# Optimization experiments

Measured on AMD Instinct MI355X. Metric: run time of the kernel, lower is better.

The kernel has to match this reference:

```python
import jax, jax.numpy as jnp
import numpy as np

EMBED_DIM = 1024
NUM_HEADS = 16
HEAD_DIM = EMBED_DIM // NUM_HEADS
B, T = 4, 2048


def setup_inputs() -> dict:
    key = jax.random.key(0)
    ks = jax.random.split(key, 11)
    s = 1.0 / np.sqrt(EMBED_DIM)
    return {
        "query": jax.random.normal(ks[0], (B, T, EMBED_DIM), jnp.float32),
        "key_in": jax.random.normal(ks[1], (B, T, EMBED_DIM), jnp.float32),
        "value": jax.random.normal(ks[2], (B, T, EMBED_DIM), jnp.float32),
        "Wq": jax.random.normal(ks[3], (EMBED_DIM, EMBED_DIM), jnp.float32) * s,
        "bq": jnp.zeros((EMBED_DIM,), jnp.float32),
        "Wk": jax.random.normal(ks[4], (EMBED_DIM, EMBED_DIM), jnp.float32) * s,
        "bk": jnp.zeros((EMBED_DIM,), jnp.float32),
        "Wv": jax.random.normal(ks[5], (EMBED_DIM, EMBED_DIM), jnp.float32) * s,
        "bv": jnp.zeros((EMBED_DIM,), jnp.float32),
        "Wo": jax.random.normal(ks[6], (EMBED_DIM, EMBED_DIM), jnp.float32) * s,
        "bo": jnp.zeros((EMBED_DIM,), jnp.float32),
    }


def reference(query, key_in, value, Wq, bq, Wk, bk, Wv, bv, Wo, bo):
    # nn.Linear: x @ W.T + b
    def split_heads(x):  # [B,T,D] -> [B,H,T,hd]
        return x.reshape(B, T, NUM_HEADS, HEAD_DIM).transpose(0, 2, 1, 3)

    q = split_heads(query @ Wq.T + bq)
    k = split_heads(key_in @ Wk.T + bk)
    v = split_heads(value @ Wv.T + bv)
    scores = jnp.einsum("bhqd,bhkd->bhqk", q, k) / jnp.sqrt(jnp.float32(HEAD_DIM))
    attn = jax.nn.softmax(scores, axis=-1)
    out = jnp.einsum("bhqk,bhkd->bhqd", attn, v)
    out = out.transpose(0, 2, 1, 3).reshape(B, T, EMBED_DIM)
    return out @ Wo.T + bo
```

## Files before the change

### kernel.cpp

```cpp
#include <hip/hip_runtime.h>
#include <hip/hip_bf16.h>
#include <stdint.h>

typedef __bf16 bf16;
typedef __bf16 bf16x8 __attribute__((ext_vector_type(8)));
typedef float f32x4 __attribute__((ext_vector_type(4)));

#define BATCH 4
#define SEQ   2048
#define DIM   1024
#define NH    16
#define HD    64

#define QSCALE 0.18033688011112042f

#define MFMA(a, b, c) __builtin_amdgcn_mfma_f32_16x16x32_bf16((a), (b), (c), 0, 0, 0)

#define GLOAD16(gsrc, ldst)                                                        \
  __builtin_amdgcn_global_load_lds(                                                \
      (__attribute__((address_space(1))) unsigned int*)(void*)(gsrc),              \
      (__attribute__((address_space(3))) unsigned int*)(ldst), 16, 0, 0)

static __device__ __forceinline__ float fast_exp2(float x) {
#if __has_builtin(__builtin_amdgcn_exp2f)
  return __builtin_amdgcn_exp2f(x);
#else
  return exp2f(x);
#endif
}

__global__ __launch_bounds__(256) void cvt_w_kernel(
    const float* __restrict__ w0, const float* __restrict__ w1,
    const float* __restrict__ w2, const float* __restrict__ w3,
    bf16* __restrict__ o0, bf16* __restrict__ o1,
    bf16* __restrict__ o2, bf16* __restrict__ o3) {
  const float* s;
  bf16* d;
  switch (blockIdx.y) {
    case 0: s = w0; d = o0; break;
    case 1: s = w1; d = o1; break;
    case 2: s = w2; d = o2; break;
    default: s = w3; d = o3; break;
  }
  const int i = (blockIdx.x * 256 + threadIdx.x) * 4;
  const float4 v = *(const float4*)(s + i);
  ushort4 o;
  o.x = __builtin_bit_cast(unsigned short, (bf16)v.x);
  o.y = __builtin_bit_cast(unsigned short, (bf16)v.y);
  o.z = __builtin_bit_cast(unsigned short, (bf16)v.z);
  o.w = __builtin_bit_cast(unsigned short, (bf16)v.w);
  *(ushort4*)((unsigned short*)d + i) = o;
}

struct ProjArgs {
  const float* A[3];
  const bf16*  W[3];
  const float* bias[3];
  bf16*        out[3];
};

__global__ __launch_bounds__(256, 3) void proj_gemm(ProjArgs p) {
  const int z = blockIdx.z;
  const float* __restrict__ A    = p.A[z];
  const bf16*  __restrict__ W    = p.W[z];
  const float* __restrict__ bias = p.bias[z];
  bf16*        __restrict__ out  = p.out[z];

  __shared__ float Af[128 * 64];
  __shared__ bf16  Bb[128 * 64];

  const int tid  = threadIdx.x;
  const int wave = tid >> 6, lane = tid & 63;
  const int r = lane & 15, g = lane >> 4;

  const int wg = blockIdx.x;
  const int sw = ((wg & 7) << 6) | (wg >> 3);
  const int m0 = (sw >> 3) * 128, n0 = (sw & 7) * 128;
  const int wm = (wave >> 1) * 64, wn = (wave & 1) * 64;

  f32x4 acc[4][4] = {};

  const int a_sr = lane >> 4;
  const int a_cb = (lane & 15) * 16;
  const int b_sr = lane >> 3;
  const int b_cb = (lane & 7) * 16;

  const int NK = DIM / 64;
  for (int it = 0; it < NK; ++it) {
    const int k0 = it * 64;

#pragma unroll
    for (int i = 0; i < 8; ++i) {
      const int row = wave * 32 + i * 4 + a_sr;
      const char* src = (const char*)(A + (size_t)(m0 + row) * DIM + k0) +
                        (a_cb ^ ((row & 15) << 4));
      GLOAD16(src, (char*)Af + (wave * 32 + i * 4) * 256);
    }
#pragma unroll
    for (int i = 0; i < 4; ++i) {
      const int row = wave * 32 + i * 8 + b_sr;
      const char* src = (const char*)(W + (size_t)(n0 + row) * DIM + k0) +
                        (b_cb ^ ((row & 7) << 4));
      GLOAD16(src, (char*)Bb + (wave * 32 + i * 8) * 128);
    }
    __syncthreads();

#pragma unroll
    for (int ks = 0; ks < 2; ++ks) {
      bf16x8 af[4], bfr[4];
#pragma unroll
      for (int mt = 0; mt < 4; ++mt) {
        const int mr = wm + mt * 16 + r;
        const char* base = (const char*)Af + mr * 256;
        const int asw = (mr & 15) << 4;
        const f32x4 lo = *(const f32x4*)(base + ((ks * 128 + g * 32) ^ asw));
        const f32x4 hi = *(const f32x4*)(base + ((ks * 128 + g * 32 + 16) ^ asw));
        bf16x8 a;
        a[0] = (bf16)lo[0]; a[1] = (bf16)lo[1]; a[2] = (bf16)lo[2]; a[3] = (bf16)lo[3];
        a[4] = (bf16)hi[0]; a[5] = (bf16)hi[1]; a[6] = (bf16)hi[2]; a[7] = (bf16)hi[3];
        af[mt] = a;
      }
#pragma unroll
      for (int nt = 0; nt < 4; ++nt) {
        const int nr = wn + nt * 16 + r;
        bfr[nt] = *(bf16x8*)((char*)Bb + nr * 128 +
                             ((ks * 64 + g * 16) ^ ((nr & 7) << 4)));
      }
#pragma unroll
      for (int mt = 0; mt < 4; ++mt)
#pragma unroll
        for (int nt = 0; nt < 4; ++nt)
          acc[mt][nt] = MFMA(af[mt], bfr[nt], acc[mt][nt]);
    }

    __syncthreads();
  }

  if (z == 2) {
#pragma unroll
    for (int nt = 0; nt < 4; ++nt) {
      const int n = n0 + wn + nt * 16 + r;
      const float bn = bias[n];
#pragma unroll
      for (int mt = 0; mt < 4; ++mt) {
        const int m = m0 + wm + mt * 16 + g * 4;
        const int b = m >> 11, t = m & 2047;
        ushort4 pk;
        pk.x = __builtin_bit_cast(unsigned short, (bf16)(acc[mt][nt][0] + bn));
        pk.y = __builtin_bit_cast(unsigned short, (bf16)(acc[mt][nt][1] + bn));
        pk.z = __builtin_bit_cast(unsigned short, (bf16)(acc[mt][nt][2] + bn));
        pk.w = __builtin_bit_cast(unsigned short, (bf16)(acc[mt][nt][3] + bn));
        *(ushort4*)((unsigned short*)out + (((size_t)(b * DIM + n)) << 11) + t) = pk;
      }
    }
  } else {
    const float scale = (z == 0) ? QSCALE : 1.0f;
#pragma unroll
    for (int mt = 0; mt < 4; ++mt)
#pragma unroll
      for (int nt = 0; nt < 4; ++nt) {
        const int n = n0 + wn + nt * 16 + r;
        const float bn = bias[n];
#pragma unroll
        for (int i = 0; i < 4; ++i) {
          const int m = m0 + wm + mt * 16 + g * 4 + i;
          out[(size_t)m * DIM + n] = (bf16)((acc[mt][nt][i] + bn) * scale);
        }
      }
  }
}

__global__ __launch_bounds__(256, 3) void attn_kernel(
    const bf16* __restrict__ Q, const bf16* __restrict__ K,
    const bf16* __restrict__ Vt, bf16* __restrict__ ctx) {
  __shared__ bf16 Kb[2][64 * 64];
  __shared__ bf16 Vb[2][64 * 64];
  __shared__ bf16 Pb[4][32 * 64];

  const int tid  = threadIdx.x;
  const int wave = tid >> 6, lane = tid & 63;
  const int r = lane & 15, g = lane >> 4;
  const int bh = blockIdx.y;
  const int b = bh >> 4, h = bh & 15;
  const int q0 = blockIdx.x * 128 + wave * 32;

  bf16x8 qf[2][2];
  {
    const bf16* qp = Q + ((size_t)(b * SEQ + q0 + r) * DIM + h * HD);
#pragma unroll
    for (int qt = 0; qt < 2; ++qt)
#pragma unroll
      for (int ks = 0; ks < 2; ++ks)
        qf[qt][ks] = *(const bf16x8*)(qp + (size_t)qt * 16 * DIM + ks * 32 + g * 8);
  }

  f32x4 accO[2][4] = {};
  float m_i[2] = {-3e38f, -3e38f};
  float l_i[2] = {0.f, 0.f};

  const bf16* Kbase = K + (size_t)(b * SEQ) * DIM + h * HD;
  const bf16* Vbase = Vt + (size_t)(b * DIM + h * HD) * SEQ;

  const int srr = lane >> 3;
  const int scb = (lane & 7) * 16;
  const int swz = srr << 4;

#define STAGE(buf, kv0)                                                             \
  do {                                                                              \
    _Pragma("unroll") for (int i_ = 0; i_ < 2; ++i_) {                              \
      const int row_ = wave * 16 + i_ * 8 + srr;                                    \
      const char* ks_ =                                                             \
          (const char*)(Kbase + (size_t)((kv0) + row_) * DIM) + (scb ^ swz);        \
      GLOAD16(ks_, (char*)&Kb[buf][0] + (wave * 16 + i_ * 8) * 128);                \
      const char* vs_ =                                                             \
          (const char*)(Vbase + (size_t)row_ * SEQ + (kv0)) + (scb ^ swz);          \
      GLOAD16(vs_, (char*)&Vb[buf][0] + (wave * 16 + i_ * 8) * 128);                \
    }                                                                               \
  } while (0)

  STAGE(0, 0);
  __syncthreads();

  const int NIT = SEQ / 64;
  for (int it = 0; it < NIT; ++it) {
    const int cur = it & 1;
    if (it + 1 < NIT) STAGE(cur ^ 1, (it + 1) * 64);

    f32x4 s[2][4];
#pragma unroll
    for (int qt = 0; qt < 2; ++qt)
#pragma unroll
      for (int nt = 0; nt < 4; ++nt) s[qt][nt] = f32x4{0.f, 0.f, 0.f, 0.f};
#pragma unroll
    for (int nt = 0; nt < 4; ++nt) {
      const int kr = nt * 16 + r;
#pragma unroll
      for (int ks = 0; ks < 2; ++ks) {
        const bf16x8 kf = *(bf16x8*)((char*)&Kb[cur][0] + kr * 128 +
                                     ((ks * 64 + g * 16) ^ ((kr & 7) << 4)));
        s[0][nt] = MFMA(kf, qf[0][ks], s[0][nt]);
        s[1][nt] = MFMA(kf, qf[1][ks], s[1][nt]);
      }
    }

    float pm[2];
#pragma unroll
    for (int qt = 0; qt < 2; ++qt) {
      f32x4 m4;
#pragma unroll
      for (int i = 0; i < 4; ++i)
        m4[i] = fmaxf(fmaxf(s[qt][0][i], s[qt][1][i]), fmaxf(s[qt][2][i], s[qt][3][i]));
      float t = fmaxf(fmaxf(m4[0], m4[1]), fmaxf(m4[2], m4[3]));
      t = fmaxf(t, __shfl_xor(t, 16));
      t = fmaxf(t, __shfl_xor(t, 32));
      pm[qt] = t;
    }

    const bool need = (pm[0] > m_i[0] + 8.0f) || (pm[1] > m_i[1] + 8.0f);
    if (__any(need)) {
      float alpha[2];
#pragma unroll
      for (int qt = 0; qt < 2; ++qt) {
        const float mn = fmaxf(m_i[qt], pm[qt]);
        alpha[qt] = fast_exp2(m_i[qt] - mn);
        m_i[qt] = mn;
        l_i[qt] *= alpha[qt];
      }
#pragma unroll
      for (int qt = 0; qt < 2; ++qt)
#pragma unroll
        for (int i = 0; i < 4; ++i) {
          const float a = __shfl(alpha[qt], g * 4 + i);
#pragma unroll
          for (int dt = 0; dt < 4; ++dt) accO[qt][dt][i] *= a;
        }
    }

    float rs[2] = {0.f, 0.f};
#pragma unroll
    for (int qt = 0; qt < 2; ++qt) {
      const int row = qt * 16 + r;
      const int rsw = (row & 7) << 4;
#pragma unroll
      for (int nt = 0; nt < 4; ++nt) {
        f32x4 pv;
#pragma unroll
        for (int i = 0; i < 4; ++i) {
          pv[i] = fast_exp2(s[qt][nt][i] - m_i[qt]);
          rs[qt] += pv[i];
        }
        ushort4 pk;
        pk.x = __builtin_bit_cast(unsigned short, (bf16)pv[0]);
        pk.y = __builtin_bit_cast(unsigned short, (bf16)pv[1]);
        pk.z = __builtin_bit_cast(unsigned short, (bf16)pv[2]);
        pk.w = __builtin_bit_cast(unsigned short, (bf16)pv[3]);
        *(ushort4*)((char*)&Pb[wave][0] + row * 128 + ((nt * 32 + g * 8) ^ rsw)) = pk;
      }
      rs[qt] += __shfl_xor(rs[qt], 16);
      rs[qt] += __shfl_xor(rs[qt], 32);
      l_i[qt] += rs[qt];
    }

#pragma unroll
    for (int ss = 0; ss < 2; ++ss) {
      bf16x8 pf[2];
#pragma unroll
      for (int qt = 0; qt < 2; ++qt) {
        const int row = qt * 16 + r;
        pf[qt] = *(bf16x8*)((char*)&Pb[wave][0] + row * 128 +
                            ((ss * 64 + g * 16) ^ ((row & 7) << 4)));
      }
#pragma unroll
      for (int dt = 0; dt < 4; ++dt) {
        const int dr = dt * 16 + r;
        const bf16x8 vf = *(bf16x8*)((char*)&Vb[cur][0] + dr * 128 +
                                     ((ss * 64 + g * 16) ^ ((dr & 7) << 4)));
        accO[0][dt] = MFMA(pf[0], vf, accO[0][dt]);
        accO[1][dt] = MFMA(pf[1], vf, accO[1][dt]);
      }
    }

    __syncthreads();
  }
#undef STAGE

#pragma unroll
  for (int qt = 0; qt < 2; ++qt)
#pragma unroll
    for (int i = 0; i < 4; ++i) {
      const float li = __shfl(l_i[qt], g * 4 + i);
      const float inv = 1.0f / li;
      const int qrow = q0 + qt * 16 + g * 4 + i;
      bf16* cp = ctx + (size_t)(b * SEQ + qrow) * DIM + h * HD;
#pragma unroll
      for (int dt = 0; dt < 4; ++dt)
        cp[dt * 16 + r] = (bf16)(accO[qt][dt][i] * inv);
    }
}

__global__ __launch_bounds__(256, 2) void out_gemm(
    const bf16* __restrict__ A, const bf16* __restrict__ W,
    const float* __restrict__ bias, float* __restrict__ out) {
  __shared__ bf16 Ab[2][128 * 64];
  __shared__ bf16 Bb[2][128 * 64];

  const int tid  = threadIdx.x;
  const int wave = tid >> 6, lane = tid & 63;
  const int r = lane & 15, g = lane >> 4;

  const int wg = blockIdx.x;
  const int sw = ((wg & 7) << 6) | (wg >> 3);
  const int m0 = (sw >> 3) * 128, n0 = (sw & 7) * 128;
  const int wm = (wave >> 1) * 64, wn = (wave & 1) * 64;

  f32x4 acc[4][4] = {};

  const int srr = lane >> 3;
  const int scb = (lane & 7) * 16;
  const int swz = srr << 4;

#define STAGE2(buf, k0)                                                             \
  do {                                                                              \
    _Pragma("unroll") for (int i_ = 0; i_ < 4; ++i_) {                              \
      const int row_ = wave * 32 + i_ * 8 + srr;                                    \
      const char* as_ =                                                             \
          (const char*)(A + (size_t)(m0 + row_) * DIM + (k0)) + (scb ^ swz);        \
      GLOAD16(as_, (char*)&Ab[buf][0] + (wave * 32 + i_ * 8) * 128);                \
      const char* bs_ =                                                             \
          (const char*)(W + (size_t)(n0 + row_) * DIM + (k0)) + (scb ^ swz);        \
      GLOAD16(bs_, (char*)&Bb[buf][0] + (wave * 32 + i_ * 8) * 128);                \
    }                                                                               \
  } while (0)

  STAGE2(0, 0);
  __syncthreads();

  const int NK = DIM / 64;
  for (int it = 0; it < NK; ++it) {
    const int cur = it & 1;
    if (it + 1 < NK) STAGE2(cur ^ 1, (it + 1) * 64);

#pragma unroll
    for (int ks = 0; ks < 2; ++ks) {
      bf16x8 af[4], bfr[4];
#pragma unroll
      for (int mt = 0; mt < 4; ++mt) {
        const int mr = wm + mt * 16 + r;
        af[mt] = *(bf16x8*)((char*)&Ab[cur][0] + mr * 128 +
                            ((ks * 64 + g * 16) ^ ((mr & 7) << 4)));
      }
#pragma unroll
      for (int nt = 0; nt < 4; ++nt) {
        const int nr = wn + nt * 16 + r;
        bfr[nt] = *(bf16x8*)((char*)&Bb[cur][0] + nr * 128 +
                             ((ks * 64 + g * 16) ^ ((nr & 7) << 4)));
      }
#pragma unroll
      for (int mt = 0; mt < 4; ++mt)
#pragma unroll
        for (int nt = 0; nt < 4; ++nt)
          acc[mt][nt] = MFMA(af[mt], bfr[nt], acc[mt][nt]);
    }

    __syncthreads();
  }
#undef STAGE2

#pragma unroll
  for (int mt = 0; mt < 4; ++mt)
#pragma unroll
    for (int nt = 0; nt < 4; ++nt) {
      const int n = n0 + wn + nt * 16 + r;
      const float bn = bias[n];
#pragma unroll
      for (int i = 0; i < 4; ++i) {
        const int m = m0 + wm + mt * 16 + g * 4 + i;
        out[(size_t)m * DIM + n] = acc[mt][nt][i] + bn;
      }
    }
}

extern "C" void kernel_launch(void* const* d_in, const int* in_sizes, int n_in,
                              void* d_out, int out_size, void* d_ws, size_t ws_size,
                              hipStream_t stream) {
  const float* query  = (const float*)d_in[0];
  const float* key_in = (const float*)d_in[1];
  const float* value  = (const float*)d_in[2];
  const float* Wq = (const float*)d_in[3];
  const float* bq = (const float*)d_in[4];
  const float* Wk = (const float*)d_in[5];
  const float* bk = (const float*)d_in[6];
  const float* Wv = (const float*)d_in[7];
  const float* bv = (const float*)d_in[8];
  const float* Wo = (const float*)d_in[9];
  const float* bo = (const float*)d_in[10];

  char* ws = (char*)d_ws;
  const size_t WSZ = (size_t)DIM * DIM * sizeof(bf16);
  const size_t TSZ = (size_t)BATCH * SEQ * DIM * sizeof(bf16);
  bf16* Wq_b = (bf16*)(ws);
  bf16* Wk_b = (bf16*)(ws + WSZ);
  bf16* Wv_b = (bf16*)(ws + 2 * WSZ);
  bf16* Wo_b = (bf16*)(ws + 3 * WSZ);
  bf16* Q_b  = (bf16*)(ws + 4 * WSZ);
  bf16* K_b  = (bf16*)(ws + 4 * WSZ + TSZ);
  bf16* Vt_b = (bf16*)(ws + 4 * WSZ + 2 * TSZ);
  bf16* C_b  = (bf16*)(ws + 4 * WSZ + 3 * TSZ);

  cvt_w_kernel<<<dim3(DIM * DIM / (256 * 4), 4), 256, 0, stream>>>(
      Wq, Wk, Wv, Wo, Wq_b, Wk_b, Wv_b, Wo_b);

  ProjArgs pa;
  pa.A[0] = query; pa.A[1] = key_in; pa.A[2] = value;
  pa.W[0] = Wq_b;  pa.W[1] = Wk_b;   pa.W[2] = Wv_b;
  pa.bias[0] = bq; pa.bias[1] = bk;  pa.bias[2] = bv;
  pa.out[0] = Q_b; pa.out[1] = K_b;  pa.out[2] = Vt_b;
  proj_gemm<<<dim3(512, 1, 3), 256, 0, stream>>>(pa);

  attn_kernel<<<dim3(SEQ / 128, BATCH * NH), 256, 0, stream>>>(Q_b, K_b, Vt_b, C_b);

  out_gemm<<<dim3(512, 1, 1), 256, 0, stream>>>(C_b, Wo_b, bo, (float*)d_out);
}
```

Before: 207.1 us.

## Switch attention to 32x32 MFMA with register-resident P and swizzled block order

The attention kernel moves from 16x16x32 to 32x32x16 bf16 MFMA and computes S transposed, so each lane owns one query row. The softmax probabilities are then fed straight from registers into the PV MFMA, which removes the per-wave P buffer in LDS along with its writes and reads. To make that register layout line up, the K rows are permuted at load time. The change also flattens the grid with an XCD-aware block swizzle, raises the occupancy hint to 4, precomputes the staging offsets, and adds s_setprio around the MFMA sections. The main risks are the correctness of the K-row permutation and higher register pressure at the new occupancy target.

```diff
diff --git a/kernel.cpp b/kernel.cpp
--- a/kernel.cpp
+++ b/kernel.cpp
@@ -5,6 +5,7 @@
 typedef __bf16 bf16;
 typedef __bf16 bf16x8 __attribute__((ext_vector_type(8)));
 typedef float f32x4 __attribute__((ext_vector_type(4)));
+typedef float f32x16 __attribute__((ext_vector_type(16)));
 
 #define BATCH 4
 #define SEQ   2048
@@ -14,7 +15,8 @@
 
 #define QSCALE 0.18033688011112042f
 
-#define MFMA(a, b, c) __builtin_amdgcn_mfma_f32_16x16x32_bf16((a), (b), (c), 0, 0, 0)
+#define MFMA(a, b, c)   __builtin_amdgcn_mfma_f32_16x16x32_bf16((a), (b), (c), 0, 0, 0)
+#define MFMA32(a, b, c) __builtin_amdgcn_mfma_f32_32x32x16_bf16((a), (b), (c), 0, 0, 0)
 
 #define GLOAD16(gsrc, ldst)                                                        \
   __builtin_amdgcn_global_load_lds(                                                \
@@ -170,33 +172,32 @@
   }
 }
 
-__global__ __launch_bounds__(256, 3) void attn_kernel(
+__global__ __launch_bounds__(256, 4) void attn_kernel(
     const bf16* __restrict__ Q, const bf16* __restrict__ K,
     const bf16* __restrict__ Vt, bf16* __restrict__ ctx) {
   __shared__ bf16 Kb[2][64 * 64];
   __shared__ bf16 Vb[2][64 * 64];
-  __shared__ bf16 Pb[4][32 * 64];
 
   const int tid  = threadIdx.x;
   const int wave = tid >> 6, lane = tid & 63;
-  const int r = lane & 15, g = lane >> 4;
-  const int bh = blockIdx.y;
+  const int l31 = lane & 31, hi = lane >> 5;
+
+  const int wg  = blockIdx.x;
+  const int swb = (wg & 7) * 128 + (wg >> 3);
+  const int qblk = swb & 15, bh = swb >> 4;
   const int b = bh >> 4, h = bh & 15;
-  const int q0 = blockIdx.x * 128 + wave * 32;
-
-  bf16x8 qf[2][2];
+  const int q0 = qblk * 128 + wave * 32;
+
+  bf16x8 qf[4];
   {
-    const bf16* qp = Q + ((size_t)(b * SEQ + q0 + r) * DIM + h * HD);
-#pragma unroll
-    for (int qt = 0; qt < 2; ++qt)
-#pragma unroll
-      for (int ks = 0; ks < 2; ++ks)
-        qf[qt][ks] = *(const bf16x8*)(qp + (size_t)qt * 16 * DIM + ks * 32 + g * 8);
-  }
-
-  f32x4 accO[2][4] = {};
-  float m_i[2] = {-3e38f, -3e38f};
-  float l_i[2] = {0.f, 0.f};
+    const bf16* qp = Q + ((size_t)(b * SEQ + q0 + l31) * DIM + h * HD);
+#pragma unroll
+    for (int st = 0; st < 4; ++st)
+      qf[st] = *(const bf16x8*)(qp + st * 16 + hi * 8);
+  }
+
+  f32x16 accO[2] = {};
+  float m_i = -3e38f, l_i = 0.0f;
 
   const bf16* Kbase = K + (size_t)(b * SEQ) * DIM + h * HD;
   const bf16* Vbase = Vt + (size_t)(b * DIM + h * HD) * SEQ;
@@ -205,16 +206,26 @@
   const int scb = (lane & 7) * 16;
   const int swz = srr << 4;
 
+  int koff[2], voff[2], kdst[2], vdst[2];
+#pragma unroll
+  for (int i = 0; i < 2; ++i) {
+    const int rl = wave * 16 + i * 8 + srr;
+    const int r32 = rl & 31;
+    const int t = (r32 >> 2) & 3;
+    const int rsrc = (rl & 32) + ((t == 1 || t == 2) ? (r32 ^ 12) : r32);
+    koff[i] = rsrc * (DIM * 2) + (scb ^ swz);
+    voff[i] = rl * (SEQ * 2) + (scb ^ swz);
+    kdst[i] = (wave * 16 + i * 8) * 128;
+    vdst[i] = (wave * 16 + i * 8) * 128;
+  }
+
 #define STAGE(buf, kv0)                                                             \
   do {                                                                              \
     _Pragma("unroll") for (int i_ = 0; i_ < 2; ++i_) {                              \
-      const int row_ = wave * 16 + i_ * 8 + srr;                                    \
-      const char* ks_ =                                                             \
-          (const char*)(Kbase + (size_t)((kv0) + row_) * DIM) + (scb ^ swz);        \
-      GLOAD16(ks_, (char*)&Kb[buf][0] + (wave * 16 + i_ * 8) * 128);                \
-      const char* vs_ =                                                             \
-          (const char*)(Vbase + (size_t)row_ * SEQ + (kv0)) + (scb ^ swz);          \
-      GLOAD16(vs_, (char*)&Vb[buf][0] + (wave * 16 + i_ * 8) * 128);                \
+      GLOAD16((const char*)Kbase + (size_t)(kv0) * (DIM * 2) + koff[i_],            \
+              (char*)&Kb[buf][0] + kdst[i_]);                                       \
+      GLOAD16((const char*)Vbase + (size_t)(kv0) * 2 + voff[i_],                    \
+              (char*)&Vb[buf][0] + vdst[i_]);                                       \
     }                                                                               \
   } while (0)
 
@@ -226,116 +237,95 @@
     const int cur = it & 1;
     if (it + 1 < NIT) STAGE(cur ^ 1, (it + 1) * 64);
 
-    f32x4 s[2][4];
-#pragma unroll
-    for (int qt = 0; qt < 2; ++qt)
-#pragma unroll
-      for (int nt = 0; nt < 4; ++nt) s[qt][nt] = f32x4{0.f, 0.f, 0.f, 0.f};
-#pragma unroll
-    for (int nt = 0; nt < 4; ++nt) {
-      const int kr = nt * 16 + r;
-#pragma unroll
-      for (int ks = 0; ks < 2; ++ks) {
-        const bf16x8 kf = *(bf16x8*)((char*)&Kb[cur][0] + kr * 128 +
-                                     ((ks * 64 + g * 16) ^ ((kr & 7) << 4)));
-        s[0][nt] = MFMA(kf, qf[0][ks], s[0][nt]);
-        s[1][nt] = MFMA(kf, qf[1][ks], s[1][nt]);
-      }
-    }
-
-    float pm[2];
-#pragma unroll
-    for (int qt = 0; qt < 2; ++qt) {
-      f32x4 m4;
-#pragma unroll
-      for (int i = 0; i < 4; ++i)
-        m4[i] = fmaxf(fmaxf(s[qt][0][i], s[qt][1][i]), fmaxf(s[qt][2][i], s[qt][3][i]));
-      float t = fmaxf(fmaxf(m4[0], m4[1]), fmaxf(m4[2], m4[3]));
-      t = fmaxf(t, __shfl_xor(t, 16));
-      t = fmaxf(t, __shfl_xor(t, 32));
-      pm[qt] = t;
-    }
-
-    const bool need = (pm[0] > m_i[0] + 8.0f) || (pm[1] > m_i[1] + 8.0f);
-    if (__any(need)) {
-      float alpha[2];
-#pragma unroll
-      for (int qt = 0; qt < 2; ++qt) {
-        const float mn = fmaxf(m_i[qt], pm[qt]);
-        alpha[qt] = fast_exp2(m_i[qt] - mn);
-        m_i[qt] = mn;
-        l_i[qt] *= alpha[qt];
-      }
-#pragma unroll
-      for (int qt = 0; qt < 2; ++qt)
-#pragma unroll
-        for (int i = 0; i < 4; ++i) {
-          const float a = __shfl(alpha[qt], g * 4 + i);
-#pragma unroll
-          for (int dt = 0; dt < 4; ++dt) accO[qt][dt][i] *= a;
+    f32x16 s[2] = {};
+    __builtin_amdgcn_s_setprio(1);
+#pragma unroll
+    for (int kvt = 0; kvt < 2; ++kvt) {
+      const int row = kvt * 32 + l31;
+      const char* kb = (const char*)&Kb[cur][0] + row * 128;
+      const int rsw = (row & 7) << 4;
+#pragma unroll
+      for (int st = 0; st < 4; ++st) {
+        const bf16x8 kf = *(const bf16x8*)(kb + ((st * 32 + hi * 16) ^ rsw));
+        s[kvt] = MFMA32(kf, qf[st], s[kvt]);
+      }
+    }
+    __builtin_amdgcn_s_setprio(0);
+
+    float pm = s[0][0];
+#pragma unroll
+    for (int kvt = 0; kvt < 2; ++kvt)
+#pragma unroll
+      for (int e = 0; e < 16; ++e)
+        if (kvt || e) pm = fmaxf(pm, s[kvt][e]);
+    pm = fmaxf(pm, __shfl_xor(pm, 32));
+
+    if (__any(pm > m_i + 8.0f)) {
+      const float mn = fmaxf(m_i, pm);
+      const float alpha = fast_exp2(m_i - mn);
+      m_i = mn;
+      l_i *= alpha;
+#pragma unroll
+      for (int dt = 0; dt < 2; ++dt)
+#pragma unroll
+        for (int e = 0; e < 16; ++e) accO[dt][e] *= alpha;
+    }
+
+    float rs = 0.0f;
+#pragma unroll
+    for (int kvt = 0; kvt < 2; ++kvt)
+#pragma unroll
+      for (int e = 0; e < 16; ++e) {
+        s[kvt][e] = fast_exp2(s[kvt][e] - m_i);
+        rs += s[kvt][e];
+      }
+    l_i += rs + __shfl_xor(rs, 32);
+
+    bf16x8 pa[2][2];
+#pragma unroll
+    for (int kvt = 0; kvt < 2; ++kvt)
+#pragma unroll
+      for (int kb = 0; kb < 2; ++kb)
+#pragma unroll
+        for (int j = 0; j < 8; ++j)
+          pa[kvt][kb][j] = (bf16)s[kvt][kb * 8 + j];
+
+    __builtin_amdgcn_s_setprio(1);
+#pragma unroll
+    for (int dt = 0; dt < 2; ++dt) {
+      const int row = dt * 32 + l31;
+      const char* vb = (const char*)&Vb[cur][0] + row * 128;
+      const int rsw = (row & 7) << 4;
+#pragma unroll
+      for (int kvt = 0; kvt < 2; ++kvt)
+#pragma unroll
+        for (int kb = 0; kb < 2; ++kb) {
+          const bf16x8 vf =
+              *(const bf16x8*)(vb + ((kvt * 64 + kb * 32 + hi * 16) ^ rsw));
+          accO[dt] = MFMA32(vf, pa[kvt][kb], accO[dt]);
         }
     }
-
-    float rs[2] = {0.f, 0.f};
-#pragma unroll
-    for (int qt = 0; qt < 2; ++qt) {
-      const int row = qt * 16 + r;
-      const int rsw = (row & 7) << 4;
-#pragma unroll
-      for (int nt = 0; nt < 4; ++nt) {
-        f32x4 pv;
-#pragma unroll
-        for (int i = 0; i < 4; ++i) {
-          pv[i] = fast_exp2(s[qt][nt][i] - m_i[qt]);
-          rs[qt] += pv[i];
-        }
+    __builtin_amdgcn_s_setprio(0);
+
+    __syncthreads();
+  }
+#undef STAGE
+
+  {
+    const float inv = 1.0f / l_i;
+    bf16* cp = ctx + (size_t)(b * SEQ + q0 + l31) * DIM + h * HD;
+#pragma unroll
+    for (int dt = 0; dt < 2; ++dt)
+#pragma unroll
+      for (int rr = 0; rr < 4; ++rr) {
         ushort4 pk;
-        pk.x = __builtin_bit_cast(unsigned short, (bf16)pv[0]);
-        pk.y = __builtin_bit_cast(unsigned short, (bf16)pv[1]);
-        pk.z = __builtin_bit_cast(unsigned short, (bf16)pv[2]);
-        pk.w = __builtin_bit_cast(unsigned short, (bf16)pv[3]);
-        *(ushort4*)((char*)&Pb[wave][0] + row * 128 + ((nt * 32 + g * 8) ^ rsw)) = pk;
-      }
-      rs[qt] += __shfl_xor(rs[qt], 16);
-      rs[qt] += __shfl_xor(rs[qt], 32);
-      l_i[qt] += rs[qt];
-    }
-
-#pragma unroll
-    for (int ss = 0; ss < 2; ++ss) {
-      bf16x8 pf[2];
-#pragma unroll
-      for (int qt = 0; qt < 2; ++qt) {
-        const int row = qt * 16 + r;
-        pf[qt] = *(bf16x8*)((char*)&Pb[wave][0] + row * 128 +
-                            ((ss * 64 + g * 16) ^ ((row & 7) << 4)));
-      }
-#pragma unroll
-      for (int dt = 0; dt < 4; ++dt) {
-        const int dr = dt * 16 + r;
-        const bf16x8 vf = *(bf16x8*)((char*)&Vb[cur][0] + dr * 128 +
-                                     ((ss * 64 + g * 16) ^ ((dr & 7) << 4)));
-        accO[0][dt] = MFMA(pf[0], vf, accO[0][dt]);
-        accO[1][dt] = MFMA(pf[1], vf, accO[1][dt]);
-      }
-    }
-
-    __syncthreads();
-  }
-#undef STAGE
-
-#pragma unroll
-  for (int qt = 0; qt < 2; ++qt)
-#pragma unroll
-    for (int i = 0; i < 4; ++i) {
-      const float li = __shfl(l_i[qt], g * 4 + i);
-      const float inv = 1.0f / li;
-      const int qrow = q0 + qt * 16 + g * 4 + i;
-      bf16* cp = ctx + (size_t)(b * SEQ + qrow) * DIM + h * HD;
-#pragma unroll
-      for (int dt = 0; dt < 4; ++dt)
-        cp[dt * 16 + r] = (bf16)(accO[qt][dt][i] * inv);
-    }
+        pk.x = __builtin_bit_cast(unsigned short, (bf16)(accO[dt][rr * 4 + 0] * inv));
+        pk.y = __builtin_bit_cast(unsigned short, (bf16)(accO[dt][rr * 4 + 1] * inv));
+        pk.z = __builtin_bit_cast(unsigned short, (bf16)(accO[dt][rr * 4 + 2] * inv));
+        pk.w = __builtin_bit_cast(unsigned short, (bf16)(accO[dt][rr * 4 + 3] * inv));
+        *(ushort4*)(cp + dt * 32 + rr * 8 + hi * 4) = pk;
+      }
+  }
 }
 
 __global__ __launch_bounds__(256, 2) void out_gemm(
@@ -457,7 +447,7 @@
   pa.out[0] = Q_b; pa.out[1] = K_b;  pa.out[2] = Vt_b;
   proj_gemm<<<dim3(512, 1, 3), 256, 0, stream>>>(pa);
 
-  attn_kernel<<<dim3(SEQ / 128, BATCH * NH), 256, 0, stream>>>(Q_b, K_b, Vt_b, C_b);
+  attn_kernel<<<dim3(1024), 256, 0, stream>>>(Q_b, K_b, Vt_b, C_b);
 
   out_gemm<<<dim3(512, 1, 1), 256, 0, stream>>>(C_b, Wo_b, bo, (float*)d_out);
 }
```

Result: faster. 182.7 us (-11.8%).
